# Kernel tuning notes

Measured on AMD Instinct MI355X. Metric: run time of the kernel, lower is better.

The kernel has to match this reference:

```python
import jax, jax.numpy as jnp
import numpy as np

N = 100_000      # nodes
E = 1_600_000    # edges
EL = 200_000     # labeled edge pairs
NODE_DIM, HID = 32, 256
H2, H4 = HID // 2, HID // 4  # 128, 64


def _lin(k, fan_in, fan_out):
    kw, kb = jax.random.split(k)
    bound = 1.0 / np.sqrt(fan_in)
    W = jax.random.uniform(kw, (fan_in, fan_out), jnp.float32, -bound, bound)
    b = jax.random.uniform(kb, (fan_out,), jnp.float32, -bound, bound)
    return W, b


def setup_inputs() -> dict:
    key = jax.random.key(0)
    ks = jax.random.split(key, 12)
    x = jax.random.normal(ks[0], (N, NODE_DIM), jnp.float32)
    edge_index = jax.random.randint(ks[1], (2, E), 0, N, jnp.int64)
    edge_label_index = jax.random.randint(ks[2], (2, EL), 0, N, jnp.int64)
    enc_w1, enc_b1 = _lin(ks[3], NODE_DIM, HID)
    enc_w2, enc_b2 = _lin(ks[4], HID, H2)
    conv_w0, conv_b0 = _lin(ks[5], H2, H4)
    conv_w1, conv_b1 = _lin(ks[6], H4, H4)
    conv_w2, conv_b2 = _lin(ks[7], H4, H4)
    ep_w1, ep_b1 = _lin(ks[8], 2 * H4, H2)
    ep_w2, ep_b2 = _lin(ks[9], H2, H4)
    ep_w3, ep_b3 = _lin(ks[10], H4, 1)
    return dict(x=x, edge_index=edge_index, edge_label_index=edge_label_index,
                enc_w1=enc_w1, enc_b1=enc_b1, enc_w2=enc_w2, enc_b2=enc_b2,
                conv_w0=conv_w0, conv_b0=conv_b0, conv_w1=conv_w1, conv_b1=conv_b1,
                conv_w2=conv_w2, conv_b2=conv_b2,
                ep_w1=ep_w1, ep_b1=ep_b1, ep_w2=ep_w2, ep_b2=ep_b2, ep_w3=ep_w3, ep_b3=ep_b3)


def reference(x, edge_index, edge_label_index,
              enc_w1, enc_b1, enc_w2, enc_b2,
              conv_w0, conv_b0, conv_w1, conv_b1, conv_w2, conv_b2,
              ep_w1, ep_b1, ep_w2, ep_b2, ep_w3, ep_b3):
    # node encoder (dropout = identity in eval)
    h = jax.nn.relu(x @ enc_w1 + enc_b1)
    h = jax.nn.relu(h @ enc_w2 + enc_b2)           # [N, 128]

    # GCN normalization with self-loops (PyG gcn_norm, edge_weight=1)
    loops = jnp.arange(N, dtype=edge_index.dtype)
    src = jnp.concatenate([edge_index[0], loops])   # [E+N]
    dst = jnp.concatenate([edge_index[1], loops])
    deg = jax.ops.segment_sum(jnp.ones(E + N, jnp.float32), dst, num_segments=N)
    dinv = jnp.where(deg > 0, jax.lax.rsqrt(jnp.maximum(deg, 1.0)), 0.0)
    norm = (dinv[src] * dinv[dst])[:, None]          # [E+N, 1]

    def gcn(h, W, b):
        xw = h @ W                                   # transform first (PyG)
        agg = jax.ops.segment_sum(xw[src] * norm, dst, num_segments=N)
        return agg + b

    for W, b in ((conv_w0, conv_b0), (conv_w1, conv_b1), (conv_w2, conv_b2)):
        h_new = jax.nn.relu(gcn(h, W, b))
        h = h + h_new if h.shape == h_new.shape else h_new
        # self.dropout -> identity in eval

    # edge predictor on labeled pairs
    ef = jnp.concatenate([h[edge_label_index[0]], h[edge_label_index[1]]], axis=1)  # [EL, 128]
    e = jax.nn.relu(ef @ ep_w1 + ep_b1)
    e = jax.nn.relu(e @ ep_w2 + ep_b2)
    e = jax.nn.sigmoid(e @ ep_w3 + ep_b3)
    return e.squeeze(-1)                             # [EL]
```

## Files before the change

kernel.cpp:

```cpp
#include <hip/hip_runtime.h>
#include <math.h>


#define N_NODES 100000
#define N_EDGES 1600000
#define N_EL    200000

#define KBUCK   98
#define WSHIFT  10
#define WMASK   1023
#define BCAP    128
#define BSTRIDE 24576
#define PART_NB 512
#define CHUNK   3125
#define LCAP    20480

typedef __attribute__((ext_vector_type(8))) short short8_t;
typedef __attribute__((ext_vector_type(4))) float f32x4;

__device__ __forceinline__ unsigned short f2bf(float f) {
    unsigned u = __float_as_uint(f);
    unsigned r = u + 0x7FFFu + ((u >> 16) & 1u);
    return (unsigned short)(r >> 16);
}

__device__ __forceinline__ float2 up16(unsigned u) {
    union { unsigned v; _Float16 h[2]; } c; c.v = u;
    return make_float2((float)c.h[0], (float)c.h[1]);
}

__global__ __launch_bounds__(256) void fill_part(const int* __restrict__ ei,
                                                 int* __restrict__ btail, int* __restrict__ bscr) {
    __shared__ int lbuf[KBUCK][BCAP];
    __shared__ int lcnt[KBUCK];
    __shared__ int offs[KBUCK + 1];
    __shared__ int gbase[KBUCK];
    int t = threadIdx.x;
    for (int i = t; i < KBUCK; i += 256) lcnt[i] = 0;
    __syncthreads();

    int e0   = blockIdx.x * CHUNK;
    int eend = e0 + CHUNK; if (eend > N_EDGES) eend = N_EDGES;
    for (int e = e0 + t; e < eend; e += 256) {
        int s = __builtin_nontemporal_load(ei + e);
        int d = __builtin_nontemporal_load(ei + N_EDGES + e);
        int b = d >> WSHIFT;
        int entry = ((d & WMASK) << 17) | s;
        int pos = atomicAdd(&lcnt[b], 1);
        if (pos < BCAP) lbuf[b][pos] = entry;
        else {
            int p = atomicAdd(&btail[b], 1);
            bscr[b * BSTRIDE + p] = entry;
        }
    }
    __syncthreads();

    if (t < KBUCK) {
        int c = lcnt[t]; if (c > BCAP) c = BCAP;
        lcnt[t] = c;
        gbase[t] = atomicAdd(&btail[t], c);
    }
    __syncthreads();
    if (t == 0) {
        offs[0] = 0;
        for (int b = 0; b < KBUCK; ++b) offs[b + 1] = offs[b] + lcnt[b];
    }
    __syncthreads();

    int T = offs[KBUCK];
    for (int i = t; i < T; i += 256) {
        int loB = 0, hiB = KBUCK;
        while (hiB - loB > 1) { int mid = (loB + hiB) >> 1; if (offs[mid] <= i) loB = mid; else hiB = mid; }
        int j = i - offs[loB];
        bscr[loB * BSTRIDE + gbase[loB] + j] = lbuf[loB][j];
    }
}

__global__ __launch_bounds__(1024) void fill_place(const int* __restrict__ btail,
                                                   const int* __restrict__ bscr,
                                                   int* __restrict__ row_ptr, float* __restrict__ dinv,
                                                   int* __restrict__ col) {
    __shared__ int ssm[128];
    __shared__ int lcnt[1024];
    __shared__ int lpre[1024];
    __shared__ int lbuf[LCAP];
    int b = blockIdx.x, t = threadIdx.x;

    if (t < 128) ssm[t] = (t < KBUCK) ? btail[t] : 0;
    lcnt[t] = 0;
    __syncthreads();
    for (int s = 1; s < 128; s <<= 1) {
        int a = 0;
        if (t < 128 && t >= s) a = ssm[t - s];
        __syncthreads();
        if (t < 128) ssm[t] += a;
        __syncthreads();
    }
    int segstart = (b == 0) ? 0 : ssm[b - 1];
    int n = btail[b];
    const int* src = bscr + b * BSTRIDE;
    for (int i = t; i < n; i += 1024)
        atomicAdd(&lcnt[src[i] >> 17], 1);
    __syncthreads();

    int c = lcnt[t];
    lpre[t] = c; __syncthreads();
    for (int s = 1; s < 1024; s <<= 1) {
        int a = (t >= s) ? lpre[t - s] : 0;
        __syncthreads();
        lpre[t] += a;
        __syncthreads();
    }
    int excl = lpre[t] - c;

    int v = (b << WSHIFT) + t;
    if (v < N_NODES) {
        row_ptr[v] = segstart + excl;
        dinv[v] = rsqrtf((float)(c + 1));
    }
    if (b == KBUCK - 1 && t == 0) row_ptr[N_NODES] = N_EDGES;
    lcnt[t] = excl;
    __syncthreads();

    if (n <= LCAP) {
        for (int i = t; i < n; i += 1024) {
            int e = src[i];
            int pos = atomicAdd(&lcnt[e >> 17], 1);
            lbuf[pos] = e & 0x1FFFF;
        }
        __syncthreads();
        for (int i = t; i < n; i += 1024)
            col[segstart + i] = lbuf[i];
    } else {
        for (int i = t; i < n; i += 1024) {
            int e = src[i];
            int pos = atomicAdd(&lcnt[e >> 17], 1);
            col[segstart + pos] = e & 0x1FFFF;
        }
    }
}

template<int KTOT, int NTOT>
__device__ __forceinline__ void wprep_one(const float* __restrict__ W, unsigned short* __restrict__ Wp, int flat) {
    if (flat >= KTOT * NTOT) return;
    int j = flat & 7, lane = (flat >> 3) & 63, kstep = (flat >> 9) & 1;
    int rest = flat >> 10;
    int ntile = rest % (NTOT / 16), chunk = rest / (NTOT / 16);
    int k = chunk * 64 + kstep * 32 + (lane >> 4) * 8 + j;
    int n = ntile * 16 + (lane & 15);
    Wp[flat] = f2bf(W[(size_t)k * NTOT + n]);
}

__device__ __forceinline__ void wprep32_one(const float* __restrict__ W, unsigned short* __restrict__ Wp, int flat) {
    if (flat >= 32 * 256) return;
    int j = flat & 7, lane = (flat >> 3) & 63, ntile = flat >> 9;
    int k = (lane >> 4) * 8 + j;
    int n = ntile * 16 + (lane & 15);
    Wp[flat] = f2bf(W[(size_t)k * 256 + n]);
}

__global__ __launch_bounds__(256) void wprep_all(
    const float* w2, const float* w0, const float* w1, const float* wpp2, const float* w1e,
    const float* wc1, const float* wc2,
    unsigned short* p2, unsigned short* p0, unsigned short* p1, unsigned short* pp2,
    unsigned short* p1e, unsigned short* pc1, unsigned short* pc2)
{
    int blk = blockIdx.x, t = threadIdx.x;
    if      (blk < 128) wprep_one<256, 128>(w2,  p2,  blk * 256 + t);
    else if (blk < 160) wprep_one<128,  64>(w0,  p0,  (blk - 128) * 256 + t);
    else if (blk < 224) wprep_one<128, 128>(w1,  p1,  (blk - 160) * 256 + t);
    else if (blk < 256) wprep_one<128,  64>(wpp2, pp2, (blk - 224) * 256 + t);
    else if (blk < 288) wprep32_one(w1e, p1e, (blk - 256) * 256 + t);
    else if (blk < 304) wprep_one< 64,  64>(wc1, pc1, (blk - 288) * 256 + t);
    else                wprep_one< 64,  64>(wc2, pc2, (blk - 304) * 256 + t);
}

__global__ __launch_bounds__(256, 3) void mfma_encfull(
    const float* __restrict__ x,
    const unsigned short* __restrict__ Wp1, const float* __restrict__ b1,
    const unsigned short* __restrict__ Wp2, const float* __restrict__ b2,
    const unsigned short* __restrict__ Wp0, const float* __restrict__ dinv,
    _Float16* __restrict__ yout, int M)
{
    __shared__ __align__(16) unsigned short smem[25088];
    unsigned short (*As)[40]   = (unsigned short(*)[40])smem;
    unsigned short* Wls1       = smem + 2560;
    unsigned short (*H1)[264]  = (unsigned short(*)[264])smem;
    unsigned short (*H128)[136]= (unsigned short(*)[136])smem;
    unsigned short* Wls2       = smem + 16896;
    unsigned short* W0s        = smem + 16896;

    int t = threadIdx.x, wave = t >> 6, lane = t & 63;
    int m0 = blockIdx.x * 64;
    int cb = lane & 15, rq = lane >> 4;

    {
        int row = t >> 2, seg = t & 3;
        int gr = m0 + row;
        float4 a = make_float4(0.f, 0.f, 0.f, 0.f), b = a;
        if (gr < M) {
            a = *(const float4*)&x[(size_t)gr * 32 + seg * 8];
            b = *(const float4*)&x[(size_t)gr * 32 + seg * 8 + 4];
        }
        unsigned short tmp[8] = { f2bf(a.x), f2bf(a.y), f2bf(a.z), f2bf(a.w),
                                  f2bf(b.x), f2bf(b.y), f2bf(b.z), f2bf(b.w) };
        *(uint4*)&As[row][seg * 8] = *(uint4*)tmp;
    }
    #pragma unroll
    for (int j = 0; j < 4; ++j)
        ((uint4*)Wls1)[t + j * 256] = ((const uint4*)Wp1)[t + j * 256];
    __syncthreads();

    short8_t af1 = *(const short8_t*)&As[wave * 16 + cb][rq * 8];
    f32x4 acc[16];
    #pragma unroll
    for (int nt = 0; nt < 16; ++nt) {
        short8_t bf = *(const short8_t*)&Wls1[(nt * 64 + lane) * 8];
        acc[nt] = __builtin_amdgcn_mfma_f32_16x16x32_bf16(af1, bf, (f32x4){0.f, 0.f, 0.f, 0.f}, 0, 0, 0);
    }
    __syncthreads();

    #pragma unroll
    for (int nt = 0; nt < 16; ++nt) {
        int col = nt * 16 + cb;
        float bv = b1[col];
        #pragma unroll
        for (int r = 0; r < 4; ++r)
            H1[wave * 16 + rq * 4 + r][col] = f2bf(fmaxf(acc[nt][r] + bv, 0.f));
    }

    f32x4 acc2[8];
    #pragma unroll
    for (int nt = 0; nt < 8; ++nt) acc2[nt] = (f32x4){0.f, 0.f, 0.f, 0.f};
    for (int ch = 0; ch < 4; ++ch) {
        #pragma unroll
        for (int j = 0; j < 4; ++j)
            ((uint4*)Wls2)[t + j * 256] = ((const uint4*)(Wp2 + (size_t)ch * 8192))[t + j * 256];
        __syncthreads();
        #pragma unroll
        for (int ks = 0; ks < 2; ++ks) {
            short8_t af = *(const short8_t*)&H1[wave * 16 + cb][ch * 64 + ks * 32 + rq * 8];
            #pragma unroll
            for (int nt = 0; nt < 8; ++nt) {
                short8_t bf = *(const short8_t*)&Wls2[((nt * 2 + ks) * 64 + lane) * 8];
                acc2[nt] = __builtin_amdgcn_mfma_f32_16x16x32_bf16(af, bf, acc2[nt], 0, 0, 0);
            }
        }
        __syncthreads();
    }

    #pragma unroll
    for (int nt = 0; nt < 8; ++nt) {
        int col = nt * 16 + cb;
        float bv = b2[col];
        #pragma unroll
        for (int r = 0; r < 4; ++r)
            H128[wave * 16 + rq * 4 + r][col] = f2bf(fmaxf(acc2[nt][r] + bv, 0.f));
    }
    ((uint4*)W0s)[t]       = ((const uint4*)Wp0)[t];
    ((uint4*)W0s)[t + 256] = ((const uint4*)Wp0)[t + 256];
    __syncthreads();

    f32x4 acc3[4];
    #pragma unroll
    for (int nt = 0; nt < 4; ++nt) acc3[nt] = (f32x4){0.f, 0.f, 0.f, 0.f};
    #pragma unroll
    for (int ch = 0; ch < 2; ++ch) {
        #pragma unroll
        for (int ks = 0; ks < 2; ++ks) {
            short8_t af = *(const short8_t*)&H128[wave * 16 + cb][ch * 64 + ks * 32 + rq * 8];
            #pragma unroll
            for (int nt = 0; nt < 4; ++nt) {
                short8_t bf = *(const short8_t*)&W0s[(((ch * 4 + nt) * 2 + ks) * 64 + lane) * 8];
                acc3[nt] = __builtin_amdgcn_mfma_f32_16x16x32_bf16(af, bf, acc3[nt], 0, 0, 0);
            }
        }
    }

    #pragma unroll
    for (int nt = 0; nt < 4; ++nt) {
        int col = nt * 16 + cb;
        #pragma unroll
        for (int r = 0; r < 4; ++r) {
            int gr = m0 + wave * 16 + rq * 4 + r;
            if (gr < M) yout[(size_t)gr * 64 + col] = (_Float16)(acc3[nt][r] * dinv[gr]);
        }
    }
}

template<int NTOT, int KTOT, bool BIAS_RELU, int OUTT>
__device__ __forceinline__ void mfma_gemm_body(
    const unsigned short* __restrict__ A, const unsigned short* __restrict__ Wp,
    const float* __restrict__ bias, const float* __restrict__ dinv,
    void* __restrict__ Cout, int M)
{
    constexpr int NT16 = NTOT / 16;
    constexpr int NCH  = KTOT / 64;
    __shared__ unsigned short As[64][72];
    __shared__ unsigned short Wls[NT16 * 1024];

    int t = threadIdx.x, wave = t >> 6, lane = t & 63;
    int m0 = blockIdx.x * 64;

    f32x4 acc[NT16];
    #pragma unroll
    for (int nt = 0; nt < NT16; ++nt) acc[nt] = (f32x4){0.f, 0.f, 0.f, 0.f};

    for (int ch = 0; ch < NCH; ++ch) {
        #pragma unroll
        for (int j = 0; j < 2; ++j) {
            int idx = t + j * 256;
            int row = idx >> 3, seg = idx & 7;
            int gr = m0 + row;
            uint4 v = make_uint4(0u, 0u, 0u, 0u);
            if (gr < M) v = *(const uint4*)(A + (size_t)gr * KTOT + ch * 64 + seg * 8);
            *(uint4*)&As[row][seg * 8] = v;
        }
        constexpr int WL16 = NT16 * 128;
        #pragma unroll
        for (int j = 0; j < WL16 / 256; ++j) {
            int idx = t + j * 256;
            ((uint4*)Wls)[idx] = ((const uint4*)(Wp + (size_t)ch * NT16 * 1024))[idx];
        }
        __syncthreads();

        #pragma unroll
        for (int ks = 0; ks < 2; ++ks) {
            short8_t af = *(const short8_t*)&As[wave * 16 + (lane & 15)][ks * 32 + (lane >> 4) * 8];
            #pragma unroll
            for (int nt = 0; nt < NT16; ++nt) {
                short8_t bf = *(const short8_t*)&Wls[((nt * 2 + ks) * 64 + lane) * 8];
                acc[nt] = __builtin_amdgcn_mfma_f32_16x16x32_bf16(af, bf, acc[nt], 0, 0, 0);
            }
        }
        __syncthreads();
    }

    int cb = lane & 15, rq = lane >> 4;
    #pragma unroll
    for (int nt = 0; nt < NT16; ++nt) {
        int col = nt * 16 + cb;
        float bv = BIAS_RELU ? bias[col] : 0.f;
        #pragma unroll
        for (int r = 0; r < 4; ++r) {
            int gr = m0 + wave * 16 + rq * 4 + r;
            if (gr < M) {
                float val;
                if (BIAS_RELU) val = fmaxf(acc[nt][r] + bv, 0.f);
                else           val = acc[nt][r] * dinv[gr];
                size_t o = (size_t)gr * NTOT + col;
                if (OUTT == 1)      ((unsigned short*)Cout)[o] = f2bf(val);
                else if (OUTT == 2) ((_Float16*)Cout)[o] = (_Float16)val;
                else                ((float*)Cout)[o] = val;
            }
        }
    }
}

__global__ __launch_bounds__(256, 4) void mfma_conv1(const unsigned short* A, const unsigned short* Wp,
                                                     const float* dinv, _Float16* C, int M) {
    mfma_gemm_body<64, 64, false, 2>(A, Wp, nullptr, dinv, C, M);
}
__global__ __launch_bounds__(256, 4) void mfma_conv2(const unsigned short* A, const unsigned short* Wp,
                                                     const float* dinv, _Float16* C, int M) {
    mfma_gemm_body<64, 64, false, 2>(A, Wp, nullptr, dinv, C, M);
}

__global__ __launch_bounds__(256, 4) void mfma_ep12(
    const unsigned short* __restrict__ A, const int* __restrict__ gidx,
    const unsigned short* __restrict__ Wp1, const float* __restrict__ b1,
    const unsigned short* __restrict__ Wp2, const float* __restrict__ b2,
    const float* __restrict__ w3, const float* __restrict__ b3,
    float* __restrict__ out, int M)
{
    __shared__ __align__(16) unsigned short smem[12800];
    unsigned short (*As)[72] = (unsigned short(*)[72])smem;
    unsigned short* Wls = smem + 4608;

    int t = threadIdx.x, wave = t >> 6, lane = t & 63;
    int m0 = blockIdx.x * 64;
    int cb = lane & 15, rq = lane >> 4;

    f32x4 acc[8];
    #pragma unroll
    for (int nt = 0; nt < 8; ++nt) acc[nt] = (f32x4){0.f, 0.f, 0.f, 0.f};

    for (int ch = 0; ch < 2; ++ch) {
        #pragma unroll
        for (int j = 0; j < 2; ++j) {
            int idx = t + j * 256;
            int row = idx >> 3, seg = idx & 7;
            int gr = m0 + row;
            uint4 v = make_uint4(0u, 0u, 0u, 0u);
            if (gr < M) {
                int node = (ch == 0) ? gidx[gr] : gidx[N_EL + gr];
                v = *(const uint4*)(A + (size_t)node * 64 + seg * 8);
            }
            *(uint4*)&As[row][seg * 8] = v;
        }
        #pragma unroll
        for (int j = 0; j < 4; ++j) {
            int idx = t + j * 256;
            ((uint4*)Wls)[idx] = ((const uint4*)(Wp1 + (size_t)ch * 8192))[idx];
        }
        __syncthreads();

        #pragma unroll
        for (int ks = 0; ks < 2; ++ks) {
            short8_t af = *(const short8_t*)&As[wave * 16 + cb][ks * 32 + rq * 8];
            #pragma unroll
            for (int nt = 0; nt < 8; ++nt) {
                short8_t bf = *(const short8_t*)&Wls[((nt * 2 + ks) * 64 + lane) * 8];
                acc[nt] = __builtin_amdgcn_mfma_f32_16x16x32_bf16(af, bf, acc[nt], 0, 0, 0);
            }
        }
        __syncthreads();
    }

    unsigned short (*E1)[136] = (unsigned short(*)[136])smem;
    unsigned short* W2s = smem + 8704;
    #pragma unroll
    for (int nt = 0; nt < 8; ++nt) {
        int col = nt * 16 + cb;
        float bv = b1[col];
        #pragma unroll
        for (int r = 0; r < 4; ++r) {
            int row = wave * 16 + rq * 4 + r;
            E1[row][col] = f2bf(fmaxf(acc[nt][r] + bv, 0.f));
        }
    }
    ((uint4*)W2s)[t]       = ((const uint4*)Wp2)[t];
    ((uint4*)W2s)[t + 256] = ((const uint4*)Wp2)[t + 256];
    __syncthreads();

    f32x4 acc2[4];
    #pragma unroll
    for (int nt = 0; nt < 4; ++nt) acc2[nt] = (f32x4){0.f, 0.f, 0.f, 0.f};
    #pragma unroll
    for (int ch = 0; ch < 2; ++ch) {
        #pragma unroll
        for (int ks = 0; ks < 2; ++ks) {
            short8_t af = *(const short8_t*)&E1[wave * 16 + cb][ch * 64 + ks * 32 + rq * 8];
            #pragma unroll
            for (int nt = 0; nt < 4; ++nt) {
                short8_t bf = *(const short8_t*)&W2s[(((ch * 4 + nt) * 2 + ks) * 64 + lane) * 8];
                acc2[nt] = __builtin_amdgcn_mfma_f32_16x16x32_bf16(af, bf, acc2[nt], 0, 0, 0);
            }
        }
    }

    float s0 = 0.f, s1 = 0.f, s2 = 0.f, s3 = 0.f;
    #pragma unroll
    for (int nt = 0; nt < 4; ++nt) {
        int col = nt * 16 + cb;
        float bv = b2[col], wv = w3[col];
        s0 += fmaxf(acc2[nt][0] + bv, 0.f) * wv;
        s1 += fmaxf(acc2[nt][1] + bv, 0.f) * wv;
        s2 += fmaxf(acc2[nt][2] + bv, 0.f) * wv;
        s3 += fmaxf(acc2[nt][3] + bv, 0.f) * wv;
    }
    #pragma unroll
    for (int off = 1; off < 16; off <<= 1) {
        s0 += __shfl_xor(s0, off);
        s1 += __shfl_xor(s1, off);
        s2 += __shfl_xor(s2, off);
        s3 += __shfl_xor(s3, off);
    }
    if (cb == 0) {
        int gr = m0 + wave * 16 + rq * 4;
        if (gr + 3 < M) {
            float bb = b3[0];
            float4 o;
            o.x = 1.f / (1.f + expf(-(s0 + bb)));
            o.y = 1.f / (1.f + expf(-(s1 + bb)));
            o.z = 1.f / (1.f + expf(-(s2 + bb)));
            o.w = 1.f / (1.f + expf(-(s3 + bb)));
            *(float4*)&out[gr] = o;
        }
    }
}

template<bool RESIDUAL, bool WF32, bool WBF16>
__device__ __forceinline__ void agg_body(
    const uint4* __restrict__ y4, const int* __restrict__ row_ptr, const int* __restrict__ col,
    const float* __restrict__ dinv, const float* __restrict__ bias,
    const float* __restrict__ hprev, float* __restrict__ hout,
    uint4* __restrict__ hb4)
{
    int v  = blockIdx.x * 32 + (threadIdx.x >> 3);
    int sl = threadIdx.x & 7;
    if (v >= N_NODES) return;

    uint4 a = y4[(size_t)v * 8 + sl];
    float2 p0 = up16(a.x), p1 = up16(a.y), p2 = up16(a.z), p3 = up16(a.w);
    float s0 = p0.x, s1 = p0.y, s2 = p1.x, s3 = p1.y;
    float s4 = p2.x, s5 = p2.y, s6 = p3.x, s7 = p3.y;

    int s = row_ptr[v], e = row_ptr[v + 1];
    int i = s;
    for (; i + 3 < e; i += 4) {
        int u0 = col[i], u1 = col[i + 1], u2 = col[i + 2], u3 = col[i + 3];
        uint4 f0 = y4[(size_t)u0 * 8 + sl];
        uint4 f1 = y4[(size_t)u1 * 8 + sl];
        uint4 f2 = y4[(size_t)u2 * 8 + sl];
        uint4 f3 = y4[(size_t)u3 * 8 + sl];
        float2 g;
        g = up16(f0.x); s0 += g.x; s1 += g.y;  g = up16(f0.y); s2 += g.x; s3 += g.y;
        g = up16(f0.z); s4 += g.x; s5 += g.y;  g = up16(f0.w); s6 += g.x; s7 += g.y;
        g = up16(f1.x); s0 += g.x; s1 += g.y;  g = up16(f1.y); s2 += g.x; s3 += g.y;
        g = up16(f1.z); s4 += g.x; s5 += g.y;  g = up16(f1.w); s6 += g.x; s7 += g.y;
        g = up16(f2.x); s0 += g.x; s1 += g.y;  g = up16(f2.y); s2 += g.x; s3 += g.y;
        g = up16(f2.z); s4 += g.x; s5 += g.y;  g = up16(f2.w); s6 += g.x; s7 += g.y;
        g = up16(f3.x); s0 += g.x; s1 += g.y;  g = up16(f3.y); s2 += g.x; s3 += g.y;
        g = up16(f3.z); s4 += g.x; s5 += g.y;  g = up16(f3.w); s6 += g.x; s7 += g.y;
    }
    for (; i < e; ++i) {
        uint4 f = y4[(size_t)col[i] * 8 + sl];
        float2 g;
        g = up16(f.x); s0 += g.x; s1 += g.y;  g = up16(f.y); s2 += g.x; s3 += g.y;
        g = up16(f.z); s4 += g.x; s5 += g.y;  g = up16(f.w); s6 += g.x; s7 += g.y;
    }

    float dv = dinv[v];
    float4 ba = *(const float4*)&bias[sl * 8];
    float4 bb = *(const float4*)&bias[sl * 8 + 4];
    float v0 = fmaxf(dv * s0 + ba.x, 0.f), v1 = fmaxf(dv * s1 + ba.y, 0.f);
    float v2 = fmaxf(dv * s2 + ba.z, 0.f), v3 = fmaxf(dv * s3 + ba.w, 0.f);
    float v4 = fmaxf(dv * s4 + bb.x, 0.f), v5 = fmaxf(dv * s5 + bb.y, 0.f);
    float v6 = fmaxf(dv * s6 + bb.z, 0.f), v7 = fmaxf(dv * s7 + bb.w, 0.f);
    if (RESIDUAL) {
        float4 h0 = *(const float4*)&hprev[(size_t)v * 64 + sl * 8];
        float4 h1 = *(const float4*)&hprev[(size_t)v * 64 + sl * 8 + 4];
        v0 += h0.x; v1 += h0.y; v2 += h0.z; v3 += h0.w;
        v4 += h1.x; v5 += h1.y; v6 += h1.z; v7 += h1.w;
    }
    if (WF32) {
        *(float4*)&hout[(size_t)v * 64 + sl * 8]     = make_float4(v0, v1, v2, v3);
        *(float4*)&hout[(size_t)v * 64 + sl * 8 + 4] = make_float4(v4, v5, v6, v7);
    }
    if (WBF16) {
        uint4 p;
        p.x = (unsigned)f2bf(v0) | ((unsigned)f2bf(v1) << 16);
        p.y = (unsigned)f2bf(v2) | ((unsigned)f2bf(v3) << 16);
        p.z = (unsigned)f2bf(v4) | ((unsigned)f2bf(v5) << 16);
        p.w = (unsigned)f2bf(v6) | ((unsigned)f2bf(v7) << 16);
        hb4[(size_t)v * 8 + sl] = p;
    }
}

__global__ __launch_bounds__(256) void agg0_kernel(const uint4* y, const int* rp, const int* col,
                                                   const float* dinv, const float* b, float* h, uint4* hb) {
    agg_body<false, true, true>(y, rp, col, dinv, b, nullptr, h, hb);
}
__global__ __launch_bounds__(256) void agg1_kernel(const uint4* y, const int* rp, const int* col,
                                                   const float* dinv, const float* b, float* h, uint4* hb) {
    agg_body<true, true, true>(y, rp, col, dinv, b, h, h, hb);
}
__global__ __launch_bounds__(256) void agg2_kernel(const uint4* y, const int* rp, const int* col,
                                                   const float* dinv, const float* b,
                                                   const float* hprev, uint4* hb) {
    agg_body<true, false, true>(y, rp, col, dinv, b, hprev, nullptr, hb);
}

extern "C" void kernel_launch(void* const* d_in, const int* in_sizes, int n_in,
                              void* d_out, int out_size, void* d_ws, size_t ws_size,
                              hipStream_t stream) {
    const float* x       = (const float*)d_in[0];
    const int*   ei      = (const int*)d_in[1];
    const int*   eli     = (const int*)d_in[2];
    const float* enc_w1  = (const float*)d_in[3];
    const float* enc_b1  = (const float*)d_in[4];
    const float* enc_w2  = (const float*)d_in[5];
    const float* enc_b2  = (const float*)d_in[6];
    const float* conv_w0 = (const float*)d_in[7];
    const float* conv_b0 = (const float*)d_in[8];
    const float* conv_w1 = (const float*)d_in[9];
    const float* conv_b1 = (const float*)d_in[10];
    const float* conv_w2 = (const float*)d_in[11];
    const float* conv_b2 = (const float*)d_in[12];
    const float* ep_w1   = (const float*)d_in[13];
    const float* ep_b1   = (const float*)d_in[14];
    const float* ep_w2   = (const float*)d_in[15];
    const float* ep_b2   = (const float*)d_in[16];
    const float* ep_w3   = (const float*)d_in[17];
    const float* ep_b3   = (const float*)d_in[18];
    float* out = (float*)d_out;

    float* fws = (float*)d_ws;
    _Float16* yb         = (_Float16*)fws;
    float* h64           = fws + 3200000;
    unsigned short* h64b = (unsigned short*)(fws + 9600000);
    int*   col     = (int*)(fws + 12800000);
    int*   row_ptr = col + 1600000;
    float* dinvp   = (float*)(row_ptr + 100032);
    unsigned short* w2p = (unsigned short*)(dinvp + 100000);
    unsigned short* w0p = w2p + 32768;
    unsigned short* w1p = w0p + 8192;
    unsigned short* wp2 = w1p + 16384;
    unsigned short* w1e = wp2 + 8192;
    unsigned short* wc1p = w1e + 8192;
    unsigned short* wc2p = wc1p + 4096;
    int*   btail   = (int*)(wc2p + 4096);
    int*   bscr    = btail + 128;

    hipMemsetAsync(btail, 0, 128 * sizeof(int), stream);
    fill_part<<<PART_NB, 256, 0, stream>>>(ei, btail, bscr);
    wprep_all<<<320, 256, 0, stream>>>(enc_w2, conv_w0, ep_w1, ep_w2, enc_w1, conv_w1, conv_w2,
                                       w2p, w0p, w1p, wp2, w1e, wc1p, wc2p);
    fill_place<<<KBUCK, 1024, 0, stream>>>(btail, bscr, row_ptr, dinvp, col);

    const int GBN = (N_NODES + 63) / 64;
    const int GBE = N_EL / 64;
    const int GBA = (N_NODES + 31) / 32;

    mfma_encfull<<<GBN, 256, 0, stream>>>(x, w1e, enc_b1, w2p, enc_b2, w0p, dinvp, yb, N_NODES);
    agg0_kernel<<<GBA, 256, 0, stream>>>((const uint4*)yb, row_ptr, col, dinvp, conv_b0, h64, (uint4*)h64b);

    mfma_conv1<<<GBN, 256, 0, stream>>>(h64b, wc1p, dinvp, yb, N_NODES);
    agg1_kernel<<<GBA, 256, 0, stream>>>((const uint4*)yb, row_ptr, col, dinvp, conv_b1, h64, (uint4*)h64b);

    mfma_conv2<<<GBN, 256, 0, stream>>>(h64b, wc2p, dinvp, yb, N_NODES);
    agg2_kernel<<<GBA, 256, 0, stream>>>((const uint4*)yb, row_ptr, col, dinvp, conv_b2, h64, (uint4*)h64b);

    mfma_ep12<<<GBE, 256, 0, stream>>>(h64b, eli, w1p, ep_b1, wp2, ep_b2, ep_w3, ep_b3, out, N_EL);
}
```

Before: 319.7 us.

## Fuse GCN aggregation with next layer's MFMA transform and merge weight prep

The aggregation kernels for layers 0 and 1 now also apply the next conv layer's 64x64 bf16 MFMA transform and the dinv scaling in-block, writing the fp16 message buffer directly. This removes the separate conv1/conv2 GEMM launches and the bf16 hidden-state round trip through global memory. Weight preparation is folded into extra blocks of the edge-partition kernel to save a launch. The fused kernels use ping-pong fp16 buffers and assume N divisible by 32 (the bounds check is dropped), and carry extra LDS and sync per block.

New measurement: 295.8 us. -7.5%, faster.

```diff
diff --git a/kernel.cpp b/kernel.cpp
--- a/kernel.cpp
+++ b/kernel.cpp
@@ -29,13 +29,50 @@
     return make_float2((float)c.h[0], (float)c.h[1]);
 }
 
+template<int KTOT, int NTOT>
+__device__ __forceinline__ void wprep_one(const float* __restrict__ W, unsigned short* __restrict__ Wp, int flat) {
+    if (flat >= KTOT * NTOT) return;
+    int j = flat & 7, lane = (flat >> 3) & 63, kstep = (flat >> 9) & 1;
+    int rest = flat >> 10;
+    int ntile = rest % (NTOT / 16), chunk = rest / (NTOT / 16);
+    int k = chunk * 64 + kstep * 32 + (lane >> 4) * 8 + j;
+    int n = ntile * 16 + (lane & 15);
+    Wp[flat] = f2bf(W[(size_t)k * NTOT + n]);
+}
+
+__device__ __forceinline__ void wprep32_one(const float* __restrict__ W, unsigned short* __restrict__ Wp, int flat) {
+    if (flat >= 32 * 256) return;
+    int j = flat & 7, lane = (flat >> 3) & 63, ntile = flat >> 9;
+    int k = (lane >> 4) * 8 + j;
+    int n = ntile * 16 + (lane & 15);
+    Wp[flat] = f2bf(W[(size_t)k * 256 + n]);
+}
+
 __global__ __launch_bounds__(256) void fill_part(const int* __restrict__ ei,
-                                                 int* __restrict__ btail, int* __restrict__ bscr) {
+                                                 int* __restrict__ btail, int* __restrict__ bscr,
+    const float* w2, const float* w0, const float* w1, const float* wpp2, const float* w1e,
+    const float* wc1, const float* wc2,
+    unsigned short* p2, unsigned short* p0, unsigned short* p1, unsigned short* pp2,
+    unsigned short* p1e, unsigned short* pc1, unsigned short* pc2)
+{
     __shared__ int lbuf[KBUCK][BCAP];
     __shared__ int lcnt[KBUCK];
     __shared__ int offs[KBUCK + 1];
     __shared__ int gbase[KBUCK];
     int t = threadIdx.x;
+
+    if (blockIdx.x >= PART_NB) {
+        int blk = blockIdx.x - PART_NB;
+        if      (blk < 128) wprep_one<256, 128>(w2,  p2,  blk * 256 + t);
+        else if (blk < 160) wprep_one<128,  64>(w0,  p0,  (blk - 128) * 256 + t);
+        else if (blk < 224) wprep_one<128, 128>(w1,  p1,  (blk - 160) * 256 + t);
+        else if (blk < 256) wprep_one<128,  64>(wpp2, pp2, (blk - 224) * 256 + t);
+        else if (blk < 288) wprep32_one(w1e, p1e, (blk - 256) * 256 + t);
+        else if (blk < 304) wprep_one< 64,  64>(wc1, pc1, (blk - 288) * 256 + t);
+        else                wprep_one< 64,  64>(wc2, pc2, (blk - 304) * 256 + t);
+        return;
+    }
+
     for (int i = t; i < KBUCK; i += 256) lcnt[i] = 0;
     __syncthreads();
 
@@ -138,41 +175,6 @@
             col[segstart + pos] = e & 0x1FFFF;
         }
     }
-}
-
-template<int KTOT, int NTOT>
-__device__ __forceinline__ void wprep_one(const float* __restrict__ W, unsigned short* __restrict__ Wp, int flat) {
-    if (flat >= KTOT * NTOT) return;
-    int j = flat & 7, lane = (flat >> 3) & 63, kstep = (flat >> 9) & 1;
-    int rest = flat >> 10;
-    int ntile = rest % (NTOT / 16), chunk = rest / (NTOT / 16);
-    int k = chunk * 64 + kstep * 32 + (lane >> 4) * 8 + j;
-    int n = ntile * 16 + (lane & 15);
-    Wp[flat] = f2bf(W[(size_t)k * NTOT + n]);
-}
-
-__device__ __forceinline__ void wprep32_one(const float* __restrict__ W, unsigned short* __restrict__ Wp, int flat) {
-    if (flat >= 32 * 256) return;
-    int j = flat & 7, lane = (flat >> 3) & 63, ntile = flat >> 9;
-    int k = (lane >> 4) * 8 + j;
-    int n = ntile * 16 + (lane & 15);
-    Wp[flat] = f2bf(W[(size_t)k * 256 + n]);
-}
-
-__global__ __launch_bounds__(256) void wprep_all(
-    const float* w2, const float* w0, const float* w1, const float* wpp2, const float* w1e,
-    const float* wc1, const float* wc2,
-    unsigned short* p2, unsigned short* p0, unsigned short* p1, unsigned short* pp2,
-    unsigned short* p1e, unsigned short* pc1, unsigned short* pc2)
-{
-    int blk = blockIdx.x, t = threadIdx.x;
-    if      (blk < 128) wprep_one<256, 128>(w2,  p2,  blk * 256 + t);
-    else if (blk < 160) wprep_one<128,  64>(w0,  p0,  (blk - 128) * 256 + t);
-    else if (blk < 224) wprep_one<128, 128>(w1,  p1,  (blk - 160) * 256 + t);
-    else if (blk < 256) wprep_one<128,  64>(wpp2, pp2, (blk - 224) * 256 + t);
-    else if (blk < 288) wprep32_one(w1e, p1e, (blk - 256) * 256 + t);
-    else if (blk < 304) wprep_one< 64,  64>(wc1, pc1, (blk - 288) * 256 + t);
-    else                wprep_one< 64,  64>(wc2, pc2, (blk - 304) * 256 + t);
 }
 
 __global__ __launch_bounds__(256, 3) void mfma_encfull(
@@ -288,208 +290,25 @@
     }
 }
 
-template<int NTOT, int KTOT, bool BIAS_RELU, int OUTT>
-__device__ __forceinline__ void mfma_gemm_body(
-    const unsigned short* __restrict__ A, const unsigned short* __restrict__ Wp,
-    const float* __restrict__ bias, const float* __restrict__ dinv,
-    void* __restrict__ Cout, int M)
-{
-    constexpr int NT16 = NTOT / 16;
-    constexpr int NCH  = KTOT / 64;
-    __shared__ unsigned short As[64][72];
-    __shared__ unsigned short Wls[NT16 * 1024];
-
-    int t = threadIdx.x, wave = t >> 6, lane = t & 63;
-    int m0 = blockIdx.x * 64;
-
-    f32x4 acc[NT16];
-    #pragma unroll
-    for (int nt = 0; nt < NT16; ++nt) acc[nt] = (f32x4){0.f, 0.f, 0.f, 0.f};
-
-    for (int ch = 0; ch < NCH; ++ch) {
-        #pragma unroll
-        for (int j = 0; j < 2; ++j) {
-            int idx = t + j * 256;
-            int row = idx >> 3, seg = idx & 7;
-            int gr = m0 + row;
-            uint4 v = make_uint4(0u, 0u, 0u, 0u);
-            if (gr < M) v = *(const uint4*)(A + (size_t)gr * KTOT + ch * 64 + seg * 8);
-            *(uint4*)&As[row][seg * 8] = v;
-        }
-        constexpr int WL16 = NT16 * 128;
-        #pragma unroll
-        for (int j = 0; j < WL16 / 256; ++j) {
-            int idx = t + j * 256;
-            ((uint4*)Wls)[idx] = ((const uint4*)(Wp + (size_t)ch * NT16 * 1024))[idx];
-        }
-        __syncthreads();
-
-        #pragma unroll
-        for (int ks = 0; ks < 2; ++ks) {
-            short8_t af = *(const short8_t*)&As[wave * 16 + (lane & 15)][ks * 32 + (lane >> 4) * 8];
-            #pragma unroll
-            for (int nt = 0; nt < NT16; ++nt) {
-                short8_t bf = *(const short8_t*)&Wls[((nt * 2 + ks) * 64 + lane) * 8];
-                acc[nt] = __builtin_amdgcn_mfma_f32_16x16x32_bf16(af, bf, acc[nt], 0, 0, 0);
-            }
-        }
-        __syncthreads();
-    }
-
-    int cb = lane & 15, rq = lane >> 4;
-    #pragma unroll
-    for (int nt = 0; nt < NT16; ++nt) {
-        int col = nt * 16 + cb;
-        float bv = BIAS_RELU ? bias[col] : 0.f;
-        #pragma unroll
-        for (int r = 0; r < 4; ++r) {
-            int gr = m0 + wave * 16 + rq * 4 + r;
-            if (gr < M) {
-                float val;
-                if (BIAS_RELU) val = fmaxf(acc[nt][r] + bv, 0.f);
-                else           val = acc[nt][r] * dinv[gr];
-                size_t o = (size_t)gr * NTOT + col;
-                if (OUTT == 1)      ((unsigned short*)Cout)[o] = f2bf(val);
-                else if (OUTT == 2) ((_Float16*)Cout)[o] = (_Float16)val;
-                else                ((float*)Cout)[o] = val;
-            }
-        }
-    }
-}
-
-__global__ __launch_bounds__(256, 4) void mfma_conv1(const unsigned short* A, const unsigned short* Wp,
-                                                     const float* dinv, _Float16* C, int M) {
-    mfma_gemm_body<64, 64, false, 2>(A, Wp, nullptr, dinv, C, M);
-}
-__global__ __launch_bounds__(256, 4) void mfma_conv2(const unsigned short* A, const unsigned short* Wp,
-                                                     const float* dinv, _Float16* C, int M) {
-    mfma_gemm_body<64, 64, false, 2>(A, Wp, nullptr, dinv, C, M);
-}
-
-__global__ __launch_bounds__(256, 4) void mfma_ep12(
-    const unsigned short* __restrict__ A, const int* __restrict__ gidx,
-    const unsigned short* __restrict__ Wp1, const float* __restrict__ b1,
-    const unsigned short* __restrict__ Wp2, const float* __restrict__ b2,
-    const float* __restrict__ w3, const float* __restrict__ b3,
-    float* __restrict__ out, int M)
-{
-    __shared__ __align__(16) unsigned short smem[12800];
-    unsigned short (*As)[72] = (unsigned short(*)[72])smem;
-    unsigned short* Wls = smem + 4608;
-
-    int t = threadIdx.x, wave = t >> 6, lane = t & 63;
-    int m0 = blockIdx.x * 64;
-    int cb = lane & 15, rq = lane >> 4;
-
-    f32x4 acc[8];
-    #pragma unroll
-    for (int nt = 0; nt < 8; ++nt) acc[nt] = (f32x4){0.f, 0.f, 0.f, 0.f};
-
-    for (int ch = 0; ch < 2; ++ch) {
-        #pragma unroll
-        for (int j = 0; j < 2; ++j) {
-            int idx = t + j * 256;
-            int row = idx >> 3, seg = idx & 7;
-            int gr = m0 + row;
-            uint4 v = make_uint4(0u, 0u, 0u, 0u);
-            if (gr < M) {
-                int node = (ch == 0) ? gidx[gr] : gidx[N_EL + gr];
-                v = *(const uint4*)(A + (size_t)node * 64 + seg * 8);
-            }
-            *(uint4*)&As[row][seg * 8] = v;
-        }
-        #pragma unroll
-        for (int j = 0; j < 4; ++j) {
-            int idx = t + j * 256;
-            ((uint4*)Wls)[idx] = ((const uint4*)(Wp1 + (size_t)ch * 8192))[idx];
-        }
-        __syncthreads();
-
-        #pragma unroll
-        for (int ks = 0; ks < 2; ++ks) {
-            short8_t af = *(const short8_t*)&As[wave * 16 + cb][ks * 32 + rq * 8];
-            #pragma unroll
-            for (int nt = 0; nt < 8; ++nt) {
-                short8_t bf = *(const short8_t*)&Wls[((nt * 2 + ks) * 64 + lane) * 8];
-                acc[nt] = __builtin_amdgcn_mfma_f32_16x16x32_bf16(af, bf, acc[nt], 0, 0, 0);
-            }
-        }
-        __syncthreads();
-    }
-
-    unsigned short (*E1)[136] = (unsigned short(*)[136])smem;
-    unsigned short* W2s = smem + 8704;
-    #pragma unroll
-    for (int nt = 0; nt < 8; ++nt) {
-        int col = nt * 16 + cb;
-        float bv = b1[col];
-        #pragma unroll
-        for (int r = 0; r < 4; ++r) {
-            int row = wave * 16 + rq * 4 + r;
-            E1[row][col] = f2bf(fmaxf(acc[nt][r] + bv, 0.f));
-        }
-    }
-    ((uint4*)W2s)[t]       = ((const uint4*)Wp2)[t];
-    ((uint4*)W2s)[t + 256] = ((const uint4*)Wp2)[t + 256];
-    __syncthreads();
-
-    f32x4 acc2[4];
-    #pragma unroll
-    for (int nt = 0; nt < 4; ++nt) acc2[nt] = (f32x4){0.f, 0.f, 0.f, 0.f};
-    #pragma unroll
-    for (int ch = 0; ch < 2; ++ch) {
-        #pragma unroll
-        for (int ks = 0; ks < 2; ++ks) {
-            short8_t af = *(const short8_t*)&E1[wave * 16 + cb][ch * 64 + ks * 32 + rq * 8];
-            #pragma unroll
-            for (int nt = 0; nt < 4; ++nt) {
-                short8_t bf = *(const short8_t*)&W2s[(((ch * 4 + nt) * 2 + ks) * 64 + lane) * 8];
-                acc2[nt] = __builtin_amdgcn_mfma_f32_16x16x32_bf16(af, bf, acc2[nt], 0, 0, 0);
-            }
-        }
-    }
-
-    float s0 = 0.f, s1 = 0.f, s2 = 0.f, s3 = 0.f;
-    #pragma unroll
-    for (int nt = 0; nt < 4; ++nt) {
-        int col = nt * 16 + cb;
-        float bv = b2[col], wv = w3[col];
-        s0 += fmaxf(acc2[nt][0] + bv, 0.f) * wv;
-        s1 += fmaxf(acc2[nt][1] + bv, 0.f) * wv;
-        s2 += fmaxf(acc2[nt][2] + bv, 0.f) * wv;
-        s3 += fmaxf(acc2[nt][3] + bv, 0.f) * wv;
-    }
-    #pragma unroll
-    for (int off = 1; off < 16; off <<= 1) {
-        s0 += __shfl_xor(s0, off);
-        s1 += __shfl_xor(s1, off);
-        s2 += __shfl_xor(s2, off);
-        s3 += __shfl_xor(s3, off);
-    }
-    if (cb == 0) {
-        int gr = m0 + wave * 16 + rq * 4;
-        if (gr + 3 < M) {
-            float bb = b3[0];
-            float4 o;
-            o.x = 1.f / (1.f + expf(-(s0 + bb)));
-            o.y = 1.f / (1.f + expf(-(s1 + bb)));
-            o.z = 1.f / (1.f + expf(-(s2 + bb)));
-            o.w = 1.f / (1.f + expf(-(s3 + bb)));
-            *(float4*)&out[gr] = o;
-        }
-    }
-}
-
-template<bool RESIDUAL, bool WF32, bool WBF16>
-__device__ __forceinline__ void agg_body(
+template<bool RESIDUAL>
+__device__ __forceinline__ void aggcv_body(
     const uint4* __restrict__ y4, const int* __restrict__ row_ptr, const int* __restrict__ col,
     const float* __restrict__ dinv, const float* __restrict__ bias,
-    const float* __restrict__ hprev, float* __restrict__ hout,
-    uint4* __restrict__ hb4)
+    const unsigned short* __restrict__ Wp,
+    float* __restrict__ h,
+    _Float16* __restrict__ yout)
 {
-    int v  = blockIdx.x * 32 + (threadIdx.x >> 3);
-    int sl = threadIdx.x & 7;
-    if (v >= N_NODES) return;
+    __shared__ __align__(16) unsigned short Ws[4096];
+    __shared__ __align__(16) unsigned short Hs[32][72];
+    __shared__ float Dv[32];
+
+    int t = threadIdx.x;
+    ((uint4*)Ws)[t]       = ((const uint4*)Wp)[t];
+    ((uint4*)Ws)[t + 256] = ((const uint4*)Wp)[t + 256];
+
+    int n  = t >> 3;
+    int sl = t & 7;
+    int v  = blockIdx.x * 32 + n;
 
     uint4 a = y4[(size_t)v * 8 + sl];
     float2 p0 = up16(a.x), p1 = up16(a.y), p2 = up16(a.z), p3 = up16(a.w);
@@ -529,37 +348,226 @@
     float v4 = fmaxf(dv * s4 + bb.x, 0.f), v5 = fmaxf(dv * s5 + bb.y, 0.f);
     float v6 = fmaxf(dv * s6 + bb.z, 0.f), v7 = fmaxf(dv * s7 + bb.w, 0.f);
     if (RESIDUAL) {
+        float4 h0 = *(const float4*)&h[(size_t)v * 64 + sl * 8];
+        float4 h1 = *(const float4*)&h[(size_t)v * 64 + sl * 8 + 4];
+        v0 += h0.x; v1 += h0.y; v2 += h0.z; v3 += h0.w;
+        v4 += h1.x; v5 += h1.y; v6 += h1.z; v7 += h1.w;
+    }
+    *(float4*)&h[(size_t)v * 64 + sl * 8]     = make_float4(v0, v1, v2, v3);
+    *(float4*)&h[(size_t)v * 64 + sl * 8 + 4] = make_float4(v4, v5, v6, v7);
+    union { unsigned short us[8]; uint4 u; } hb;
+    hb.us[0] = f2bf(v0); hb.us[1] = f2bf(v1); hb.us[2] = f2bf(v2); hb.us[3] = f2bf(v3);
+    hb.us[4] = f2bf(v4); hb.us[5] = f2bf(v5); hb.us[6] = f2bf(v6); hb.us[7] = f2bf(v7);
+    *(uint4*)&Hs[n][sl * 8] = hb.u;
+    if (sl == 0) Dv[n] = dv;
+    __syncthreads();
+
+    int wave = t >> 6, lane = t & 63;
+    int rt   = wave & 1;
+    int ct0  = (wave >> 1) * 2;
+    f32x4 acc0 = (f32x4){0.f, 0.f, 0.f, 0.f}, acc1 = acc0;
+    #pragma unroll
+    for (int ks = 0; ks < 2; ++ks) {
+        short8_t af = *(const short8_t*)&Hs[rt * 16 + (lane & 15)][ks * 32 + (lane >> 4) * 8];
+        short8_t b0 = *(const short8_t*)&Ws[((ct0 * 2 + ks) * 64 + lane) * 8];
+        short8_t b1 = *(const short8_t*)&Ws[(((ct0 + 1) * 2 + ks) * 64 + lane) * 8];
+        acc0 = __builtin_amdgcn_mfma_f32_16x16x32_bf16(af, b0, acc0, 0, 0, 0);
+        acc1 = __builtin_amdgcn_mfma_f32_16x16x32_bf16(af, b1, acc1, 0, 0, 0);
+    }
+    int cb = lane & 15, rq = lane >> 4;
+    #pragma unroll
+    for (int r = 0; r < 4; ++r) {
+        int row = rt * 16 + rq * 4 + r;
+        float dv2 = Dv[row];
+        size_t go = (size_t)(blockIdx.x * 32 + row) * 64;
+        yout[go + ct0 * 16 + cb]       = (_Float16)(acc0[r] * dv2);
+        yout[go + (ct0 + 1) * 16 + cb] = (_Float16)(acc1[r] * dv2);
+    }
+}
+
+__global__ __launch_bounds__(256, 6) void aggcv0_kernel(
+    const uint4* y, const int* rp, const int* col, const float* dinv, const float* b,
+    const unsigned short* Wp, float* h, _Float16* yout) {
+    aggcv_body<false>(y, rp, col, dinv, b, Wp, h, yout);
+}
+__global__ __launch_bounds__(256, 6) void aggcv1_kernel(
+    const uint4* y, const int* rp, const int* col, const float* dinv, const float* b,
+    const unsigned short* Wp, float* h, _Float16* yout) {
+    aggcv_body<true>(y, rp, col, dinv, b, Wp, h, yout);
+}
+
+__global__ __launch_bounds__(256) void agg2_kernel(
+    const uint4* __restrict__ y4, const int* __restrict__ row_ptr, const int* __restrict__ col,
+    const float* __restrict__ dinv, const float* __restrict__ bias,
+    const float* __restrict__ hprev, uint4* __restrict__ hb4)
+{
+    int v  = blockIdx.x * 32 + (threadIdx.x >> 3);
+    int sl = threadIdx.x & 7;
+    if (v >= N_NODES) return;
+
+    uint4 a = y4[(size_t)v * 8 + sl];
+    float2 p0 = up16(a.x), p1 = up16(a.y), p2 = up16(a.z), p3 = up16(a.w);
+    float s0 = p0.x, s1 = p0.y, s2 = p1.x, s3 = p1.y;
+    float s4 = p2.x, s5 = p2.y, s6 = p3.x, s7 = p3.y;
+
+    int s = row_ptr[v], e = row_ptr[v + 1];
+    int i = s;
+    for (; i + 3 < e; i += 4) {
+        int u0 = col[i], u1 = col[i + 1], u2 = col[i + 2], u3 = col[i + 3];
+        uint4 f0 = y4[(size_t)u0 * 8 + sl];
+        uint4 f1 = y4[(size_t)u1 * 8 + sl];
+        uint4 f2 = y4[(size_t)u2 * 8 + sl];
+        uint4 f3 = y4[(size_t)u3 * 8 + sl];
+        float2 g;
+        g = up16(f0.x); s0 += g.x; s1 += g.y;  g = up16(f0.y); s2 += g.x; s3 += g.y;
+        g = up16(f0.z); s4 += g.x; s5 += g.y;  g = up16(f0.w); s6 += g.x; s7 += g.y;
+        g = up16(f1.x); s0 += g.x; s1 += g.y;  g = up16(f1.y); s2 += g.x; s3 += g.y;
+        g = up16(f1.z); s4 += g.x; s5 += g.y;  g = up16(f1.w); s6 += g.x; s7 += g.y;
+        g = up16(f2.x); s0 += g.x; s1 += g.y;  g = up16(f2.y); s2 += g.x; s3 += g.y;
+        g = up16(f2.z); s4 += g.x; s5 += g.y;  g = up16(f2.w); s6 += g.x; s7 += g.y;
+        g = up16(f3.x); s0 += g.x; s1 += g.y;  g = up16(f3.y); s2 += g.x; s3 += g.y;
+        g = up16(f3.z); s4 += g.x; s5 += g.y;  g = up16(f3.w); s6 += g.x; s7 += g.y;
+    }
+    for (; i < e; ++i) {
+        uint4 f = y4[(size_t)col[i] * 8 + sl];
+        float2 g;
+        g = up16(f.x); s0 += g.x; s1 += g.y;  g = up16(f.y); s2 += g.x; s3 += g.y;
+        g = up16(f.z); s4 += g.x; s5 += g.y;  g = up16(f.w); s6 += g.x; s7 += g.y;
+    }
+
+    float dv = dinv[v];
+    float4 ba = *(const float4*)&bias[sl * 8];
+    float4 bb = *(const float4*)&bias[sl * 8 + 4];
+    float v0 = fmaxf(dv * s0 + ba.x, 0.f), v1 = fmaxf(dv * s1 + ba.y, 0.f);
+    float v2 = fmaxf(dv * s2 + ba.z, 0.f), v3 = fmaxf(dv * s3 + ba.w, 0.f);
+    float v4 = fmaxf(dv * s4 + bb.x, 0.f), v5 = fmaxf(dv * s5 + bb.y, 0.f);
+    float v6 = fmaxf(dv * s6 + bb.z, 0.f), v7 = fmaxf(dv * s7 + bb.w, 0.f);
+    {
         float4 h0 = *(const float4*)&hprev[(size_t)v * 64 + sl * 8];
         float4 h1 = *(const float4*)&hprev[(size_t)v * 64 + sl * 8 + 4];
         v0 += h0.x; v1 += h0.y; v2 += h0.z; v3 += h0.w;
         v4 += h1.x; v5 += h1.y; v6 += h1.z; v7 += h1.w;
     }
-    if (WF32) {
-        *(float4*)&hout[(size_t)v * 64 + sl * 8]     = make_float4(v0, v1, v2, v3);
-        *(float4*)&hout[(size_t)v * 64 + sl * 8 + 4] = make_float4(v4, v5, v6, v7);
-    }
-    if (WBF16) {
-        uint4 p;
-        p.x = (unsigned)f2bf(v0) | ((unsigned)f2bf(v1) << 16);
-        p.y = (unsigned)f2bf(v2) | ((unsigned)f2bf(v3) << 16);
-        p.z = (unsigned)f2bf(v4) | ((unsigned)f2bf(v5) << 16);
-        p.w = (unsigned)f2bf(v6) | ((unsigned)f2bf(v7) << 16);
-        hb4[(size_t)v * 8 + sl] = p;
-    }
-}
-
-__global__ __launch_bounds__(256) void agg0_kernel(const uint4* y, const int* rp, const int* col,
-                                                   const float* dinv, const float* b, float* h, uint4* hb) {
-    agg_body<false, true, true>(y, rp, col, dinv, b, nullptr, h, hb);
-}
-__global__ __launch_bounds__(256) void agg1_kernel(const uint4* y, const int* rp, const int* col,
-                                                   const float* dinv, const float* b, float* h, uint4* hb) {
-    agg_body<true, true, true>(y, rp, col, dinv, b, h, h, hb);
-}
-__global__ __launch_bounds__(256) void agg2_kernel(const uint4* y, const int* rp, const int* col,
-                                                   const float* dinv, const float* b,
-                                                   const float* hprev, uint4* hb) {
-    agg_body<true, false, true>(y, rp, col, dinv, b, hprev, nullptr, hb);
+    uint4 p;
+    p.x = (unsigned)f2bf(v0) | ((unsigned)f2bf(v1) << 16);
+    p.y = (unsigned)f2bf(v2) | ((unsigned)f2bf(v3) << 16);
+    p.z = (unsigned)f2bf(v4) | ((unsigned)f2bf(v5) << 16);
+    p.w = (unsigned)f2bf(v6) | ((unsigned)f2bf(v7) << 16);
+    hb4[(size_t)v * 8 + sl] = p;
+}
+
+__global__ __launch_bounds__(256, 4) void mfma_ep12(
+    const unsigned short* __restrict__ A, const int* __restrict__ gidx,
+    const unsigned short* __restrict__ Wp1, const float* __restrict__ b1,
+    const unsigned short* __restrict__ Wp2, const float* __restrict__ b2,
+    const float* __restrict__ w3, const float* __restrict__ b3,
+    float* __restrict__ out, int M)
+{
+    __shared__ __align__(16) unsigned short smem[12800];
+    unsigned short (*As)[72] = (unsigned short(*)[72])smem;
+    unsigned short* Wls = smem + 4608;
+
+    int t = threadIdx.x, wave = t >> 6, lane = t & 63;
+    int m0 = blockIdx.x * 64;
+    int cb = lane & 15, rq = lane >> 4;
+
+    f32x4 acc[8];
+    #pragma unroll
+    for (int nt = 0; nt < 8; ++nt) acc[nt] = (f32x4){0.f, 0.f, 0.f, 0.f};
+
+    for (int ch = 0; ch < 2; ++ch) {
+        #pragma unroll
+        for (int j = 0; j < 2; ++j) {
+            int idx = t + j * 256;
+            int row = idx >> 3, seg = idx & 7;
+            int gr = m0 + row;
+            uint4 v = make_uint4(0u, 0u, 0u, 0u);
+            if (gr < M) {
+                int node = (ch == 0) ? gidx[gr] : gidx[N_EL + gr];
+                v = *(const uint4*)(A + (size_t)node * 64 + seg * 8);
+            }
+            *(uint4*)&As[row][seg * 8] = v;
+        }
+        #pragma unroll
+        for (int j = 0; j < 4; ++j) {
+            int idx = t + j * 256;
+            ((uint4*)Wls)[idx] = ((const uint4*)(Wp1 + (size_t)ch * 8192))[idx];
+        }
+        __syncthreads();
+
+        #pragma unroll
+        for (int ks = 0; ks < 2; ++ks) {
+            short8_t af = *(const short8_t*)&As[wave * 16 + cb][ks * 32 + rq * 8];
+            #pragma unroll
+            for (int nt = 0; nt < 8; ++nt) {
+                short8_t bf = *(const short8_t*)&Wls[((nt * 2 + ks) * 64 + lane) * 8];
+                acc[nt] = __builtin_amdgcn_mfma_f32_16x16x32_bf16(af, bf, acc[nt], 0, 0, 0);
+            }
+        }
+        __syncthreads();
+    }
+
+    unsigned short (*E1)[136] = (unsigned short(*)[136])smem;
+    unsigned short* W2s = smem + 8704;
+    #pragma unroll
+    for (int nt = 0; nt < 8; ++nt) {
+        int col = nt * 16 + cb;
+        float bv = b1[col];
+        #pragma unroll
+        for (int r = 0; r < 4; ++r) {
+            int row = wave * 16 + rq * 4 + r;
+            E1[row][col] = f2bf(fmaxf(acc[nt][r] + bv, 0.f));
+        }
+    }
+    ((uint4*)W2s)[t]       = ((const uint4*)Wp2)[t];
+    ((uint4*)W2s)[t + 256] = ((const uint4*)Wp2)[t + 256];
+    __syncthreads();
+
+    f32x4 acc2[4];
+    #pragma unroll
+    for (int nt = 0; nt < 4; ++nt) acc2[nt] = (f32x4){0.f, 0.f, 0.f, 0.f};
+    #pragma unroll
+    for (int ch = 0; ch < 2; ++ch) {
+        #pragma unroll
+        for (int ks = 0; ks < 2; ++ks) {
+            short8_t af = *(const short8_t*)&E1[wave * 16 + cb][ch * 64 + ks * 32 + rq * 8];
+            #pragma unroll
+            for (int nt = 0; nt < 4; ++nt) {
+                short8_t bf = *(const short8_t*)&W2s[(((ch * 4 + nt) * 2 + ks) * 64 + lane) * 8];
+                acc2[nt] = __builtin_amdgcn_mfma_f32_16x16x32_bf16(af, bf, acc2[nt], 0, 0, 0);
+            }
+        }
+    }
+
+    float s0 = 0.f, s1 = 0.f, s2 = 0.f, s3 = 0.f;
+    #pragma unroll
+    for (int nt = 0; nt < 4; ++nt) {
+        int col = nt * 16 + cb;
+        float bv = b2[col], wv = w3[col];
+        s0 += fmaxf(acc2[nt][0] + bv, 0.f) * wv;
+        s1 += fmaxf(acc2[nt][1] + bv, 0.f) * wv;
+        s2 += fmaxf(acc2[nt][2] + bv, 0.f) * wv;
+        s3 += fmaxf(acc2[nt][3] + bv, 0.f) * wv;
+    }
+    #pragma unroll
+    for (int off = 1; off < 16; off <<= 1) {
+        s0 += __shfl_xor(s0, off);
+        s1 += __shfl_xor(s1, off);
+        s2 += __shfl_xor(s2, off);
+        s3 += __shfl_xor(s3, off);
+    }
+    if (cb == 0) {
+        int gr = m0 + wave * 16 + rq * 4;
+        if (gr + 3 < M) {
+            float bb = b3[0];
+            float4 o;
+            o.x = 1.f / (1.f + expf(-(s0 + bb)));
+            o.y = 1.f / (1.f + expf(-(s1 + bb)));
+            o.z = 1.f / (1.f + expf(-(s2 + bb)));
+            o.w = 1.f / (1.f + expf(-(s3 + bb)));
+            *(float4*)&out[gr] = o;
+        }
+    }
 }
 
 extern "C" void kernel_launch(void* const* d_in, const int* in_sizes, int n_in,
@@ -603,24 +611,26 @@
     int*   btail   = (int*)(wc2p + 4096);
     int*   bscr    = btail + 128;
 
+    _Float16* yb2 = (_Float16*)h64b;
+
     hipMemsetAsync(btail, 0, 128 * sizeof(int), stream);
-    fill_part<<<PART_NB, 256, 0, stream>>>(ei, btail, bscr);
-    wprep_all<<<320, 256, 0, stream>>>(enc_w2, conv_w0, ep_w1, ep_w2, enc_w1, conv_w1, conv_w2,
-                                       w2p, w0p, w1p, wp2, w1e, wc1p, wc2p);
+    fill_part<<<PART_NB + 320, 256, 0, stream>>>(ei, btail, bscr,
+        enc_w2, conv_w0, ep_w1, ep_w2, enc_w1, conv_w1, conv_w2,
+        w2p, w0p, w1p, wp2, w1e, wc1p, wc2p);
     fill_place<<<KBUCK, 1024, 0, stream>>>(btail, bscr, row_ptr, dinvp, col);
 
     const int GBN = (N_NODES + 63) / 64;
     const int GBE = N_EL / 64;
-    const int GBA = (N_NODES + 31) / 32;
+    const int GBA = N_NODES / 32;
 
     mfma_encfull<<<GBN, 256, 0, stream>>>(x, w1e, enc_b1, w2p, enc_b2, w0p, dinvp, yb, N_NODES);
-    agg0_kernel<<<GBA, 256, 0, stream>>>((const uint4*)yb, row_ptr, col, dinvp, conv_b0, h64, (uint4*)h64b);
-
-    mfma_conv1<<<GBN, 256, 0, stream>>>(h64b, wc1p, dinvp, yb, N_NODES);
-    agg1_kernel<<<GBA, 256, 0, stream>>>((const uint4*)yb, row_ptr, col, dinvp, conv_b1, h64, (uint4*)h64b);
-
-    mfma_conv2<<<GBN, 256, 0, stream>>>(h64b, wc2p, dinvp, yb, N_NODES);
-    agg2_kernel<<<GBA, 256, 0, stream>>>((const uint4*)yb, row_ptr, col, dinvp, conv_b2, h64, (uint4*)h64b);
+
+    aggcv0_kernel<<<GBA, 256, 0, stream>>>((const uint4*)yb, row_ptr, col, dinvp, conv_b0,
+                                           wc1p, h64, yb2);
+    aggcv1_kernel<<<GBA, 256, 0, stream>>>((const uint4*)yb2, row_ptr, col, dinvp, conv_b1,
+                                           wc2p, h64, yb);
+    agg2_kernel<<<GBA, 256, 0, stream>>>((const uint4*)yb, row_ptr, col, dinvp, conv_b2,
+                                         h64, (uint4*)h64b);
 
     mfma_ep12<<<GBE, 256, 0, stream>>>(h64b, eli, w1p, ep_b1, wp2, ep_b2, ep_w3, ep_b3, out, N_EL);
 }
```
